# Kernel tuning notes

Measured on AMD Instinct MI355X. Metric: run time of the kernel, lower is better.

## Reference

```python
import jax, jax.numpy as jnp
import numpy as np

TOP_K = 2
POOL = 4  # EfficientSpatialRouter.pool_scale


def silu(v):
    return v * jax.nn.sigmoid(v)


def setup_inputs() -> dict:
    key = jax.random.key(0)
    ks = jax.random.split(key, 6)
    B, C, H, W = 16, 256, 56, 56
    E, O = 4, 256
    hidden = 2 * C            # SimpleExpert expand_ratio=2
    red = max(C // 8, 8)      # router reduced_channels
    x = jax.random.normal(ks[0], (B, C, H, W), jnp.float32)
    router_w1 = jax.random.normal(ks[1], (red, C, 3, 3), jnp.float32) * 0.02
    router_w2 = jax.random.normal(ks[2], (E, red), jnp.float32) * 0.01
    expert_w1 = jax.random.normal(ks[3], (E, hidden, C), jnp.float32) * 0.05
    expert_w2 = jax.random.normal(ks[4], (E, O, hidden), jnp.float32) * 0.03
    shared_w = jax.random.normal(ks[5], (O, C), jnp.float32) * 0.05
    return {"x": x, "router_w1": router_w1, "router_w2": router_w2,
            "expert_w1": expert_w1, "expert_w2": expert_w2, "shared_w": shared_w}


def reference(x, router_w1, router_w2, expert_w1, expert_w2, shared_w):
    # Eval mode: no router noise; BatchNorm with default running stats
    # (mean=0, var=1, gamma=1, beta=0) is the identity, so BNs are omitted.
    B, C, H, W = x.shape
    E = router_w2.shape[0]

    # --- EfficientSpatialRouter ---
    xp = x.reshape(B, C, H // POOL, POOL, W // POOL, POOL).mean(axis=(3, 5))
    h = jax.lax.conv_general_dilated(
        xp, router_w1, window_strides=(1, 1), padding=((1, 1), (1, 1)),
        dimension_numbers=("NCHW", "OIHW", "NCHW"))
    h = silu(h)  # [B, red, H/4, W/4]
    # 1x1 conv to E channels then spatial mean == mean of per-pixel logits
    logits = jnp.einsum("er,brij->be", router_w2, h) / (h.shape[2] * h.shape[3])
    probs = jax.nn.softmax(logits, axis=1)
    topv, topi = jax.lax.top_k(probs, TOP_K)          # [B,k]
    topv = topv / (topv.sum(axis=1, keepdims=True) + 1e-6)

    # --- shared expert (1x1 conv + BN(id) + SiLU) ---
    shared = silu(jnp.einsum("oc,bcij->boij", shared_w, x))

    # --- all SimpleExperts densely (1x1 conv -> SiLU -> 1x1 conv) ---
    hid = silu(jnp.einsum("edc,bcij->bedij", expert_w1, x))   # [B,E,hid,H,W]
    eo = jnp.einsum("eod,bedij->beoij", expert_w2, hid)       # [B,E,O,H,W]

    # --- weighted combine of top-k experts ---
    wdense = jnp.zeros((B, E), x.dtype).at[jnp.arange(B)[:, None], topi].add(topv)
    expert_out = jnp.einsum("be,beoij->boij", wdense, eo)
    return shared + expert_out
```

## Files before the change

### kernel.cpp

```cpp
#include <hip/hip_runtime.h>
#include <hip/hip_bf16.h>

typedef __attribute__((ext_vector_type(8))) short bf16x8;
typedef __attribute__((ext_vector_type(16))) float f32x16;
typedef __attribute__((ext_vector_type(4))) unsigned short ushort4v;

static __device__ __forceinline__ unsigned short f2bf(float f) {
  unsigned u = __float_as_uint(f);
  return (unsigned short)((u + 0x7FFFu + ((u >> 16) & 1u)) >> 16);
}
static __device__ __forceinline__ float silu_f(float v) { return v / (1.f + __expf(-v)); }

#define MFMA32(a, b, c) __builtin_amdgcn_mfma_f32_32x32x16_bf16((a), (b), (c), 0, 0, 0)

__global__ void prep_k(const float* __restrict__ shw, const float* __restrict__ ew1,
                       const float* __restrict__ ew2, const float* __restrict__ x,
                       unsigned short* __restrict__ wshp, unsigned short* __restrict__ w1p,
                       unsigned short* __restrict__ w2p, float* __restrict__ xp) {
  const int bid = blockIdx.x;
  if (bid < 4352) {
    int idx = bid * 256 + threadIdx.x;
    if (idx < 65536) {
      int j = idx;
      int i = j & 7, l = (j >> 3) & 63, ks = (j >> 9) & 15, rb = j >> 13;
      int row = rb * 32 + (l & 31), k = ks * 16 + (l >> 5) * 8 + i;
      wshp[j] = f2bf(shw[row * 256 + k]);
    } else if (idx < 589824) {
      int j = idx - 65536;
      int i = j & 7, l = (j >> 3) & 63, ks = (j >> 9) & 15, rb = (j >> 13) & 15, e = j >> 17;
      int row = rb * 32 + (l & 31), k = ks * 16 + (l >> 5) * 8 + i;
      w1p[j] = f2bf(ew1[((size_t)e * 512 + row) * 256 + k]);
    } else if (idx < 1114112) {
      int j = idx - 589824;
      int i = j & 7, l = (j >> 3) & 63, ks = (j >> 9) & 31, rb = (j >> 14) & 7, e = j >> 17;
      int row = rb * 32 + (l & 31), k = ks * 16 + (l >> 5) * 8 + i;
      w2p[j] = f2bf(ew2[((size_t)e * 256 + row) * 512 + k]);
    }
  } else {
    int idx = (bid - 4352) * 256 + threadIdx.x;
    if (idx >= 16 * 256 * 196) return;
    int pj = idx % 14, tmp = idx / 14, pi = tmp % 14, bc = tmp / 14;
    const float* src = x + (size_t)bc * 3136 + pi * 4 * 56 + pj * 4;
    float s = 0.f;
#pragma unroll
    for (int u = 0; u < 4; ++u) {
      float4 v = *reinterpret_cast<const float4*>(src + u * 56);
      s += v.x + v.y + v.z + v.w;
    }
    xp[idx] = s * 0.0625f;
  }
}

__global__ __launch_bounds__(256) void router_conv_k(const float* __restrict__ xp,
                                                     const float* __restrict__ rw1,
                                                     float* __restrict__ hsum) {
  const int b = blockIdx.x >> 5, r = blockIdx.x & 31;
  __shared__ float wl[2304];
  __shared__ float xl[32][256];
  __shared__ float red[4][196];
  __shared__ float red2[4];
  const int t = threadIdx.x;
  const int w = t >> 6, l = t & 63;
  for (int i = t; i < 2304; i += 256) wl[i] = rw1[r * 2304 + i];
  for (int i = t; i < 32 * 256; i += 256) (&xl[0][0])[i] = 0.f;
  const int ui = (l < 49) ? (l / 7) : 0, uj = (l < 49) ? (l % 7) : 0;
  float acc[4] = {0.f, 0.f, 0.f, 0.f};
  for (int cc = 0; cc < 8; ++cc) {
    __syncthreads();
    for (int i = t; i < 32 * 196; i += 256) {
      int c = i / 196, px = i % 196;
      xl[c][(px / 14 + 1) * 16 + (px % 14 + 1)] =
          xp[((size_t)b * 256 + cc * 32 + c) * 196 + px];
    }
    __syncthreads();
    if (l < 49) {
#pragma unroll 2
      for (int ci = 0; ci < 8; ++ci) {
        const int c = w * 8 + ci;
        float xv[4][4];
        const float* xb = &xl[c][ui * 32 + uj * 2];
#pragma unroll
        for (int dr = 0; dr < 4; ++dr)
#pragma unroll
          for (int dc = 0; dc < 4; ++dc) xv[dr][dc] = xb[dr * 16 + dc];
        const float* wp = &wl[(cc * 32 + c) * 9];
        float wv[9];
#pragma unroll
        for (int j = 0; j < 9; ++j) wv[j] = wp[j];
#pragma unroll
        for (int di = 0; di < 2; ++di)
#pragma unroll
          for (int dj = 0; dj < 2; ++dj) {
            float a = acc[di * 2 + dj];
#pragma unroll
            for (int du = 0; du < 3; ++du)
#pragma unroll
              for (int dv = 0; dv < 3; ++dv)
                a += xv[di + du][dj + dv] * wv[du * 3 + dv];
            acc[di * 2 + dj] = a;
          }
      }
    }
  }
  if (l < 49) {
#pragma unroll
    for (int k = 0; k < 4; ++k) red[w][(ui * 7 + uj) * 4 + k] = acc[k];
  }
  __syncthreads();
  float s = 0.f;
  if (t < 196) {
    float tot = red[0][t] + red[1][t] + red[2][t] + red[3][t];
    s = silu_f(tot);
  }
#pragma unroll
  for (int off = 32; off > 0; off >>= 1) s += __shfl_down(s, off);
  if ((t & 63) == 0) red2[t >> 6] = s;
  __syncthreads();
  if (t == 0) hsum[b * 32 + r] = red2[0] + red2[1] + red2[2] + red2[3];
}

__global__ void topk_k(const float* __restrict__ hsum, const float* __restrict__ rw2,
                       float* __restrict__ selv, int* __restrict__ sele) {
  const int t = threadIdx.x;
  const int b = t >> 2, e = t & 3;
  float l = 0.f;
#pragma unroll
  for (int r = 0; r < 32; ++r) l += rw2[e * 32 + r] * hsum[b * 32 + r];
  l *= (1.f / 196.f);
  float m = fmaxf(l, __shfl_xor(l, 1));
  m = fmaxf(m, __shfl_xor(m, 2));
  float p = __expf(l - m);
  float sm = p + __shfl_xor(p, 1);
  sm += __shfl_xor(sm, 2);
  float prob = p / sm;
  float p0 = __shfl(prob, (b << 2) | 0);
  float p1 = __shfl(prob, (b << 2) | 1);
  float p2 = __shfl(prob, (b << 2) | 2);
  float p3 = __shfl(prob, (b << 2) | 3);
  if (e == 0) {
    float pr[4] = {p0, p1, p2, p3};
    int i1 = 0;
    for (int i = 1; i < 4; ++i)
      if (pr[i] > pr[i1]) i1 = i;
    int i2 = (i1 == 0) ? 1 : 0;
    for (int i = 0; i < 4; ++i) {
      if (i == i1 || i == i2) continue;
      if (pr[i] > pr[i2]) i2 = i;
    }
    float denom = pr[i1] + pr[i2] + 1e-6f;
    selv[b * 2 + 0] = pr[i1] / denom;
    selv[b * 2 + 1] = pr[i2] / denom;
    sele[b * 2 + 0] = i1;
    sele[b * 2 + 1] = i2;
  }
}

template <int NKS>
static __device__ __forceinline__ void gemm_rf2(
    const unsigned short* __restrict__ A0, const unsigned short* __restrict__ A1,
    const unsigned short* B0, const unsigned short* B1, f32x16 acc[2][2]) {
#pragma unroll
  for (int kk = 0; kk < NKS; ++kk) {
    const bf16x8 a0 = *reinterpret_cast<const bf16x8*>(A0 + kk * 512);
    const bf16x8 a1 = *reinterpret_cast<const bf16x8*>(A1 + kk * 512);
    const bf16x8 b0 = *reinterpret_cast<const bf16x8*>(B0 + kk * 1024);
    const bf16x8 b1 = *reinterpret_cast<const bf16x8*>(B1 + kk * 1024);
    acc[0][0] = MFMA32(a0, b0, acc[0][0]);
    acc[0][1] = MFMA32(a0, b1, acc[0][1]);
    acc[1][0] = MFMA32(a1, b0, acc[1][0]);
    acc[1][1] = MFMA32(a1, b1, acc[1][1]);
  }
}

__global__ __launch_bounds__(256, 2) void moe_main_k(
    const float* __restrict__ x, const unsigned short* __restrict__ wshp,
    const unsigned short* __restrict__ w1p, const unsigned short* __restrict__ w2p,
    const float* __restrict__ selv, const int* __restrict__ sele,
    float* __restrict__ out) {
  constexpr int HW = 3136;
  __shared__ __align__(16) unsigned short xs[32 * 64 * 8];
  __shared__ __align__(16) unsigned short hs[2][16 * 64 * 8];

  const int b = blockIdx.x / 49, tile = blockIdx.x - b * 49;
  const int px0 = tile * 64;
  const int t = threadIdx.x;
  const int w = t >> 6, l = t & 63;
  const int l31 = l & 31, lh = l >> 5;

  {
    const float* xb = x + (size_t)b * 256 * HW + px0 + l;
#pragma unroll
    for (int cg = 0; cg < 8; ++cg) {
      const int c0 = w * 64 + cg * 8;
      alignas(16) unsigned short tmp[8];
#pragma unroll
      for (int i = 0; i < 8; ++i) tmp[i] = f2bf(xb[(size_t)(c0 + i) * HW]);
      *reinterpret_cast<bf16x8*>(&xs[((c0 >> 3) * 64 + l) * 8]) =
          *reinterpret_cast<const bf16x8*>(tmp);
    }
  }

  const unsigned short* xB0 = xs + (lh * 64 + l31) * 8;
  const unsigned short* xB1 = xB0 + 256;

  const int e0 = sele[b * 2 + 0], e1 = sele[b * 2 + 1];
  const float v0 = selv[b * 2 + 0], v1 = selv[b * 2 + 1];

  f32x16 oacc[2][2];
  f32x16 hacc[2];
#pragma unroll
  for (int i = 0; i < 2; ++i)
#pragma unroll
    for (int j = 0; j < 2; ++j)
#pragma unroll
      for (int r = 0; r < 16; ++r) oacc[i][j][r] = 0.f;
#pragma unroll
  for (int j = 0; j < 2; ++j)
#pragma unroll
    for (int r = 0; r < 16; ++r) hacc[j][r] = 0.f;

  __syncthreads();

  {
    const unsigned short* A1 = w1p + (size_t)((e0 * 16 + w) * 16) * 512 + l * 8;
    const unsigned short* As = wshp + (size_t)(w * 2) * 16 * 512 + l * 8;
#pragma unroll
    for (int kk = 0; kk < 16; ++kk) {
      const bf16x8 a1 = *reinterpret_cast<const bf16x8*>(A1 + kk * 512);
      const bf16x8 s0 = *reinterpret_cast<const bf16x8*>(As + kk * 512);
      const bf16x8 s1 = *reinterpret_cast<const bf16x8*>(As + 8192 + kk * 512);
      const bf16x8 b0 = *reinterpret_cast<const bf16x8*>(xB0 + kk * 1024);
      const bf16x8 b1 = *reinterpret_cast<const bf16x8*>(xB1 + kk * 1024);
      hacc[0] = MFMA32(a1, b0, hacc[0]);
      hacc[1] = MFMA32(a1, b1, hacc[1]);
      oacc[0][0] = MFMA32(s0, b0, oacc[0][0]);
      oacc[0][1] = MFMA32(s0, b1, oacc[0][1]);
      oacc[1][0] = MFMA32(s1, b0, oacc[1][0]);
      oacc[1][1] = MFMA32(s1, b1, oacc[1][1]);
    }
  }
#pragma unroll
  for (int i = 0; i < 2; ++i)
#pragma unroll
    for (int j = 0; j < 2; ++j)
#pragma unroll
      for (int r = 0; r < 16; ++r) oacc[i][j][r] = silu_f(oacc[i][j][r]);

#pragma unroll
  for (int cf = 0; cf < 2; ++cf)
#pragma unroll
    for (int g = 0; g < 4; ++g) {
      alignas(8) unsigned short pk[4];
#pragma unroll
      for (int j = 0; j < 4; ++j) pk[j] = f2bf(v0 * silu_f(hacc[cf][g * 4 + j]));
      const int ui2 = ((w * 4 + g) * 64 + cf * 32 + l31) * 8 + lh * 4;
      *reinterpret_cast<ushort4v*>(&hs[0][ui2]) = *reinterpret_cast<const ushort4v*>(pk);
    }
  __syncthreads();

#pragma unroll 1
  for (int p = 1; p < 8; ++p) {
    const int e = (p >> 2) ? e1 : e0, ch = p & 3;
    const int ep = ((p - 1) >> 2) ? e1 : e0, chp = (p - 1) & 3;
    const float v = (p >> 2) ? v1 : v0;
    const unsigned short* A1 = w1p + (size_t)((e * 16 + ch * 4 + w) * 16) * 512 + l * 8;
    const unsigned short* A2 = w2p + ((size_t)(ep * 8 + w * 2) * 32 + chp * 8) * 512 + l * 8;
    const unsigned short* B2 = hs[(p - 1) & 1] + (lh * 64 + l31) * 8;
#pragma unroll
    for (int j = 0; j < 2; ++j)
#pragma unroll
      for (int r = 0; r < 16; ++r) hacc[j][r] = 0.f;
#pragma unroll
    for (int kk = 0; kk < 16; ++kk) {
      const bf16x8 a1 = *reinterpret_cast<const bf16x8*>(A1 + kk * 512);
      const bf16x8 b0 = *reinterpret_cast<const bf16x8*>(xB0 + kk * 1024);
      const bf16x8 b1 = *reinterpret_cast<const bf16x8*>(xB1 + kk * 1024);
      hacc[0] = MFMA32(a1, b0, hacc[0]);
      hacc[1] = MFMA32(a1, b1, hacc[1]);
      if ((kk & 1) == 0) {
        const int ks2 = kk >> 1;
        const bf16x8 a20 = *reinterpret_cast<const bf16x8*>(A2 + ks2 * 512);
        const bf16x8 a21 = *reinterpret_cast<const bf16x8*>(A2 + 16384 + ks2 * 512);
        const bf16x8 h0 = *reinterpret_cast<const bf16x8*>(B2 + ks2 * 1024);
        const bf16x8 h1 = *reinterpret_cast<const bf16x8*>(B2 + 256 + ks2 * 1024);
        oacc[0][0] = MFMA32(a20, h0, oacc[0][0]);
        oacc[0][1] = MFMA32(a20, h1, oacc[0][1]);
        oacc[1][0] = MFMA32(a21, h0, oacc[1][0]);
        oacc[1][1] = MFMA32(a21, h1, oacc[1][1]);
      }
    }
#pragma unroll
    for (int cf = 0; cf < 2; ++cf)
#pragma unroll
      for (int g = 0; g < 4; ++g) {
        alignas(8) unsigned short pk[4];
#pragma unroll
        for (int j = 0; j < 4; ++j) pk[j] = f2bf(v * silu_f(hacc[cf][g * 4 + j]));
        const int ui2 = ((w * 4 + g) * 64 + cf * 32 + l31) * 8 + lh * 4;
        *reinterpret_cast<ushort4v*>(&hs[p & 1][ui2]) =
            *reinterpret_cast<const ushort4v*>(pk);
      }
    __syncthreads();
  }

  {
    const unsigned short* A2 = w2p + ((size_t)(e1 * 8 + w * 2) * 32 + 3 * 8) * 512 + l * 8;
    const unsigned short* B2 = hs[1] + (lh * 64 + l31) * 8;
    gemm_rf2<8>(A2, A2 + 16384, B2, B2 + 256, oacc);
  }

#pragma unroll
  for (int rfi = 0; rfi < 2; ++rfi)
#pragma unroll
    for (int cf = 0; cf < 2; ++cf)
#pragma unroll
      for (int r = 0; r < 16; ++r) {
        const int o = w * 64 + rfi * 32 + (r & 3) + 8 * (r >> 2) + 4 * lh;
        out[((size_t)b * 256 + o) * HW + px0 + cf * 32 + l31] = oacc[rfi][cf][r];
      }
}

extern "C" void kernel_launch(void* const* d_in, const int* in_sizes, int n_in,
                              void* d_out, int out_size, void* d_ws, size_t ws_size,
                              hipStream_t stream) {
  const float* x = (const float*)d_in[0];
  const float* rw1 = (const float*)d_in[1];
  const float* rw2 = (const float*)d_in[2];
  const float* ew1 = (const float*)d_in[3];
  const float* ew2 = (const float*)d_in[4];
  const float* shw = (const float*)d_in[5];
  float* out = (float*)d_out;
  char* ws = (char*)d_ws;

  float* xp = (float*)(ws);
  float* hsum = (float*)(ws + 3211264);
  float* selv = (float*)(ws + 3213312);
  int* sele = (int*)(ws + 3213440);
  unsigned short* wshp = (unsigned short*)(ws + 3213568);
  unsigned short* w1p = wshp + 65536;
  unsigned short* w2p = w1p + 524288;

  prep_k<<<7488, 256, 0, stream>>>(shw, ew1, ew2, x, wshp, w1p, w2p, xp);
  router_conv_k<<<512, 256, 0, stream>>>(xp, rw1, hsum);
  topk_k<<<1, 64, 0, stream>>>(hsum, rw2, selv, sele);
  moe_main_k<<<784, 256, 0, stream>>>(x, wshp, w1p, w2p, selv, sele, out);
}
```

Measured before the change: 188.7 us.

## Warp-specialize MoE main kernel into producer and consumer wave groups

Splits the four waves of each block into two roles. Two producer waves compute the expert hidden activations (first expert GEMM plus SiLU) into a single shared buffer. Two consumer waves compute the shared expert and accumulate the second expert GEMM over a 128-row output slice, and the two groups hand off through paired barriers. It also raises launch bounds to 3 blocks per SM, halves the hidden LDS buffer, and adds s_setprio around MFMA bursts. The intent is to overlap the two GEMM stages across waves and raise occupancy, at the cost of larger per-wave accumulators (register pressure) and a possible load imbalance between the roles.

```diff
diff --git a/kernel.cpp b/kernel.cpp
--- a/kernel.cpp
+++ b/kernel.cpp
@@ -155,31 +155,14 @@
   }
 }
 
-template <int NKS>
-static __device__ __forceinline__ void gemm_rf2(
-    const unsigned short* __restrict__ A0, const unsigned short* __restrict__ A1,
-    const unsigned short* B0, const unsigned short* B1, f32x16 acc[2][2]) {
-#pragma unroll
-  for (int kk = 0; kk < NKS; ++kk) {
-    const bf16x8 a0 = *reinterpret_cast<const bf16x8*>(A0 + kk * 512);
-    const bf16x8 a1 = *reinterpret_cast<const bf16x8*>(A1 + kk * 512);
-    const bf16x8 b0 = *reinterpret_cast<const bf16x8*>(B0 + kk * 1024);
-    const bf16x8 b1 = *reinterpret_cast<const bf16x8*>(B1 + kk * 1024);
-    acc[0][0] = MFMA32(a0, b0, acc[0][0]);
-    acc[0][1] = MFMA32(a0, b1, acc[0][1]);
-    acc[1][0] = MFMA32(a1, b0, acc[1][0]);
-    acc[1][1] = MFMA32(a1, b1, acc[1][1]);
-  }
-}
-
-__global__ __launch_bounds__(256, 2) void moe_main_k(
+__global__ __launch_bounds__(256, 3) void moe_main_k(
     const float* __restrict__ x, const unsigned short* __restrict__ wshp,
     const unsigned short* __restrict__ w1p, const unsigned short* __restrict__ w2p,
     const float* __restrict__ selv, const int* __restrict__ sele,
     float* __restrict__ out) {
   constexpr int HW = 3136;
   __shared__ __align__(16) unsigned short xs[32 * 64 * 8];
-  __shared__ __align__(16) unsigned short hs[2][16 * 64 * 8];
+  __shared__ __align__(16) unsigned short hs[16 * 64 * 8];
 
   const int b = blockIdx.x / 49, tile = blockIdx.x - b * 49;
   const int px0 = tile * 64;
@@ -202,122 +185,161 @@
 
   const unsigned short* xB0 = xs + (lh * 64 + l31) * 8;
   const unsigned short* xB1 = xB0 + 256;
+  const unsigned short* hB0 = hs + (lh * 64 + l31) * 8;
+  const unsigned short* hB1 = hB0 + 256;
 
   const int e0 = sele[b * 2 + 0], e1 = sele[b * 2 + 1];
   const float v0 = selv[b * 2 + 0], v1 = selv[b * 2 + 1];
 
-  f32x16 oacc[2][2];
-  f32x16 hacc[2];
-#pragma unroll
-  for (int i = 0; i < 2; ++i)
-#pragma unroll
-    for (int j = 0; j < 2; ++j)
-#pragma unroll
-      for (int r = 0; r < 16; ++r) oacc[i][j][r] = 0.f;
-#pragma unroll
-  for (int j = 0; j < 2; ++j)
-#pragma unroll
-    for (int r = 0; r < 16; ++r) hacc[j][r] = 0.f;
-
   __syncthreads();
 
-  {
-    const unsigned short* A1 = w1p + (size_t)((e0 * 16 + w) * 16) * 512 + l * 8;
-    const unsigned short* As = wshp + (size_t)(w * 2) * 16 * 512 + l * 8;
-#pragma unroll
-    for (int kk = 0; kk < 16; ++kk) {
-      const bf16x8 a1 = *reinterpret_cast<const bf16x8*>(A1 + kk * 512);
-      const bf16x8 s0 = *reinterpret_cast<const bf16x8*>(As + kk * 512);
-      const bf16x8 s1 = *reinterpret_cast<const bf16x8*>(As + 8192 + kk * 512);
-      const bf16x8 b0 = *reinterpret_cast<const bf16x8*>(xB0 + kk * 1024);
-      const bf16x8 b1 = *reinterpret_cast<const bf16x8*>(xB1 + kk * 1024);
-      hacc[0] = MFMA32(a1, b0, hacc[0]);
-      hacc[1] = MFMA32(a1, b1, hacc[1]);
-      oacc[0][0] = MFMA32(s0, b0, oacc[0][0]);
-      oacc[0][1] = MFMA32(s0, b1, oacc[0][1]);
-      oacc[1][0] = MFMA32(s1, b0, oacc[1][0]);
-      oacc[1][1] = MFMA32(s1, b1, oacc[1][1]);
-    }
-  }
-#pragma unroll
-  for (int i = 0; i < 2; ++i)
-#pragma unroll
-    for (int j = 0; j < 2; ++j)
-#pragma unroll
-      for (int r = 0; r < 16; ++r) oacc[i][j][r] = silu_f(oacc[i][j][r]);
-
-#pragma unroll
-  for (int cf = 0; cf < 2; ++cf)
-#pragma unroll
-    for (int g = 0; g < 4; ++g) {
-      alignas(8) unsigned short pk[4];
-#pragma unroll
-      for (int j = 0; j < 4; ++j) pk[j] = f2bf(v0 * silu_f(hacc[cf][g * 4 + j]));
-      const int ui2 = ((w * 4 + g) * 64 + cf * 32 + l31) * 8 + lh * 4;
-      *reinterpret_cast<ushort4v*>(&hs[0][ui2]) = *reinterpret_cast<const ushort4v*>(pk);
-    }
-  __syncthreads();
-
+  if (w < 2) {
+    f32x16 hacc[2][2];
 #pragma unroll 1
-  for (int p = 1; p < 8; ++p) {
-    const int e = (p >> 2) ? e1 : e0, ch = p & 3;
-    const int ep = ((p - 1) >> 2) ? e1 : e0, chp = (p - 1) & 3;
-    const float v = (p >> 2) ? v1 : v0;
-    const unsigned short* A1 = w1p + (size_t)((e * 16 + ch * 4 + w) * 16) * 512 + l * 8;
-    const unsigned short* A2 = w2p + ((size_t)(ep * 8 + w * 2) * 32 + chp * 8) * 512 + l * 8;
-    const unsigned short* B2 = hs[(p - 1) & 1] + (lh * 64 + l31) * 8;
-#pragma unroll
-    for (int j = 0; j < 2; ++j)
-#pragma unroll
-      for (int r = 0; r < 16; ++r) hacc[j][r] = 0.f;
-#pragma unroll
-    for (int kk = 0; kk < 16; ++kk) {
-      const bf16x8 a1 = *reinterpret_cast<const bf16x8*>(A1 + kk * 512);
-      const bf16x8 b0 = *reinterpret_cast<const bf16x8*>(xB0 + kk * 1024);
-      const bf16x8 b1 = *reinterpret_cast<const bf16x8*>(xB1 + kk * 1024);
-      hacc[0] = MFMA32(a1, b0, hacc[0]);
-      hacc[1] = MFMA32(a1, b1, hacc[1]);
-      if ((kk & 1) == 0) {
-        const int ks2 = kk >> 1;
-        const bf16x8 a20 = *reinterpret_cast<const bf16x8*>(A2 + ks2 * 512);
-        const bf16x8 a21 = *reinterpret_cast<const bf16x8*>(A2 + 16384 + ks2 * 512);
-        const bf16x8 h0 = *reinterpret_cast<const bf16x8*>(B2 + ks2 * 1024);
-        const bf16x8 h1 = *reinterpret_cast<const bf16x8*>(B2 + 256 + ks2 * 1024);
-        oacc[0][0] = MFMA32(a20, h0, oacc[0][0]);
-        oacc[0][1] = MFMA32(a20, h1, oacc[0][1]);
-        oacc[1][0] = MFMA32(a21, h0, oacc[1][0]);
-        oacc[1][1] = MFMA32(a21, h1, oacc[1][1]);
-      }
-    }
-#pragma unroll
-    for (int cf = 0; cf < 2; ++cf)
-#pragma unroll
-      for (int g = 0; g < 4; ++g) {
-        alignas(8) unsigned short pk[4];
-#pragma unroll
-        for (int j = 0; j < 4; ++j) pk[j] = f2bf(v * silu_f(hacc[cf][g * 4 + j]));
-        const int ui2 = ((w * 4 + g) * 64 + cf * 32 + l31) * 8 + lh * 4;
-        *reinterpret_cast<ushort4v*>(&hs[p & 1][ui2]) =
-            *reinterpret_cast<const ushort4v*>(pk);
-      }
+    for (int p = 0; p < 8; ++p) {
+      const int e = (p >> 2) ? e1 : e0;
+      const float v = (p >> 2) ? v1 : v0;
+      const unsigned short* A1 =
+          w1p + (size_t)((e * 16 + (p & 3) * 4 + w * 2) * 16) * 512 + l * 8;
+#pragma unroll
+      for (int i = 0; i < 2; ++i)
+#pragma unroll
+        for (int j = 0; j < 2; ++j)
+#pragma unroll
+          for (int r = 0; r < 16; ++r) hacc[i][j][r] = 0.f;
+#pragma unroll
+      for (int kk = 0; kk < 16; ++kk) {
+        const bf16x8 a0 = *reinterpret_cast<const bf16x8*>(A1 + kk * 512);
+        const bf16x8 a1 = *reinterpret_cast<const bf16x8*>(A1 + 8192 + kk * 512);
+        const bf16x8 b0 = *reinterpret_cast<const bf16x8*>(xB0 + kk * 1024);
+        const bf16x8 b1 = *reinterpret_cast<const bf16x8*>(xB1 + kk * 1024);
+        __builtin_amdgcn_s_setprio(1);
+        hacc[0][0] = MFMA32(a0, b0, hacc[0][0]);
+        hacc[0][1] = MFMA32(a0, b1, hacc[0][1]);
+        hacc[1][0] = MFMA32(a1, b0, hacc[1][0]);
+        hacc[1][1] = MFMA32(a1, b1, hacc[1][1]);
+        __builtin_amdgcn_s_setprio(0);
+      }
+      ushort4v pk[2][2][4];
+#pragma unroll
+      for (int rfi = 0; rfi < 2; ++rfi)
+#pragma unroll
+        for (int cf = 0; cf < 2; ++cf)
+#pragma unroll
+          for (int g = 0; g < 4; ++g) {
+            alignas(8) unsigned short tmp[4];
+#pragma unroll
+            for (int j = 0; j < 4; ++j)
+              tmp[j] = f2bf(v * silu_f(hacc[rfi][cf][g * 4 + j]));
+            pk[rfi][cf][g] = *reinterpret_cast<const ushort4v*>(tmp);
+          }
+      __syncthreads();
+#pragma unroll
+      for (int rfi = 0; rfi < 2; ++rfi)
+#pragma unroll
+        for (int cf = 0; cf < 2; ++cf)
+#pragma unroll
+          for (int g = 0; g < 4; ++g) {
+            const int kg = w * 8 + rfi * 4 + g;
+            const int ui2 = (kg * 64 + cf * 32 + l31) * 8 + lh * 4;
+            *reinterpret_cast<ushort4v*>(&hs[ui2]) = pk[rfi][cf][g];
+          }
+      __syncthreads();
+    }
+  } else {
+    const int wc = w - 2;
+    f32x16 oacc[4][2];
+#pragma unroll
+    for (int i = 0; i < 4; ++i)
+#pragma unroll
+      for (int j = 0; j < 2; ++j)
+#pragma unroll
+        for (int r = 0; r < 16; ++r) oacc[i][j][r] = 0.f;
+
+    {
+      const unsigned short* As = wshp + (size_t)((wc * 4) * 16) * 512 + l * 8;
+#pragma unroll
+      for (int kk = 0; kk < 16; ++kk) {
+        bf16x8 a[4];
+#pragma unroll
+        for (int rr = 0; rr < 4; ++rr)
+          a[rr] = *reinterpret_cast<const bf16x8*>(As + rr * 8192 + kk * 512);
+        const bf16x8 b0 = *reinterpret_cast<const bf16x8*>(xB0 + kk * 1024);
+        const bf16x8 b1 = *reinterpret_cast<const bf16x8*>(xB1 + kk * 1024);
+        __builtin_amdgcn_s_setprio(1);
+#pragma unroll
+        for (int rr = 0; rr < 4; ++rr) {
+          oacc[rr][0] = MFMA32(a[rr], b0, oacc[rr][0]);
+          oacc[rr][1] = MFMA32(a[rr], b1, oacc[rr][1]);
+        }
+        __builtin_amdgcn_s_setprio(0);
+      }
+    }
+#pragma unroll
+    for (int i = 0; i < 4; ++i)
+#pragma unroll
+      for (int j = 0; j < 2; ++j)
+#pragma unroll
+        for (int r = 0; r < 16; ++r) oacc[i][j][r] = silu_f(oacc[i][j][r]);
+
     __syncthreads();
-  }
-
-  {
-    const unsigned short* A2 = w2p + ((size_t)(e1 * 8 + w * 2) * 32 + 3 * 8) * 512 + l * 8;
-    const unsigned short* B2 = hs[1] + (lh * 64 + l31) * 8;
-    gemm_rf2<8>(A2, A2 + 16384, B2, B2 + 256, oacc);
-  }
-
-#pragma unroll
-  for (int rfi = 0; rfi < 2; ++rfi)
-#pragma unroll
-    for (int cf = 0; cf < 2; ++cf)
-#pragma unroll
-      for (int r = 0; r < 16; ++r) {
-        const int o = w * 64 + rfi * 32 + (r & 3) + 8 * (r >> 2) + 4 * lh;
-        out[((size_t)b * 256 + o) * HW + px0 + cf * 32 + l31] = oacc[rfi][cf][r];
-      }
+    __syncthreads();
+
+#pragma unroll 1
+    for (int p = 1; p < 8; ++p) {
+      const int q = p - 1;
+      const int e = (q >> 2) ? e1 : e0;
+      const unsigned short* A2 =
+          w2p + ((size_t)(e * 8 + wc * 4) * 32 + (q & 3) * 8) * 512 + l * 8;
+#pragma unroll
+      for (int kk = 0; kk < 8; ++kk) {
+        bf16x8 a[4];
+#pragma unroll
+        for (int rr = 0; rr < 4; ++rr)
+          a[rr] = *reinterpret_cast<const bf16x8*>(A2 + rr * 16384 + kk * 512);
+        const bf16x8 h0 = *reinterpret_cast<const bf16x8*>(hB0 + kk * 1024);
+        const bf16x8 h1 = *reinterpret_cast<const bf16x8*>(hB1 + kk * 1024);
+        __builtin_amdgcn_s_setprio(1);
+#pragma unroll
+        for (int rr = 0; rr < 4; ++rr) {
+          oacc[rr][0] = MFMA32(a[rr], h0, oacc[rr][0]);
+          oacc[rr][1] = MFMA32(a[rr], h1, oacc[rr][1]);
+        }
+        __builtin_amdgcn_s_setprio(0);
+      }
+      __syncthreads();
+      __syncthreads();
+    }
+
+    {
+      const unsigned short* A2 =
+          w2p + ((size_t)(e1 * 8 + wc * 4) * 32 + 3 * 8) * 512 + l * 8;
+#pragma unroll
+      for (int kk = 0; kk < 8; ++kk) {
+        bf16x8 a[4];
+#pragma unroll
+        for (int rr = 0; rr < 4; ++rr)
+          a[rr] = *reinterpret_cast<const bf16x8*>(A2 + rr * 16384 + kk * 512);
+        const bf16x8 h0 = *reinterpret_cast<const bf16x8*>(hB0 + kk * 1024);
+        const bf16x8 h1 = *reinterpret_cast<const bf16x8*>(hB1 + kk * 1024);
+#pragma unroll
+        for (int rr = 0; rr < 4; ++rr) {
+          oacc[rr][0] = MFMA32(a[rr], h0, oacc[rr][0]);
+          oacc[rr][1] = MFMA32(a[rr], h1, oacc[rr][1]);
+        }
+      }
+    }
+
+#pragma unroll
+    for (int rr = 0; rr < 4; ++rr)
+#pragma unroll
+      for (int cf = 0; cf < 2; ++cf)
+#pragma unroll
+        for (int r = 0; r < 16; ++r) {
+          const int o = wc * 128 + rr * 32 + (r & 3) + 8 * (r >> 2) + 4 * lh;
+          out[((size_t)b * 256 + o) * HW + px0 + cf * 32 + l31] = oacc[rr][cf][r];
+        }
+  }
 }
 
 extern "C" void kernel_launch(void* const* d_in, const int* in_sizes, int n_in,
```

After: 247.7 us. 1.31x slower.

## Hold x fragments in registers, alias smem, and software-pipeline weight loads

Applied to the files above, without the earlier changes.

Loads the block's whole bf16 x tile from LDS into registers once (32 bf16x8 fragments per lane), so the x staging buffer can be reused as the hidden buffer and shared memory drops to 32KB. The pipeline that overlapped GEMM1 of one phase with GEMM2 of the previous phase through a double-buffered hs is replaced by sequential GEMM1 then GEMM2 per phase. Each phase now has an extra barrier, and weight loads are explicitly prefetched with s_setprio and sched_barrier hints. The large register footprint risks spilling or lower occupancy under launch_bounds(256,2), and the cross-phase overlap is lost.

```diff
diff --git a/kernel.cpp b/kernel.cpp
--- a/kernel.cpp
+++ b/kernel.cpp
@@ -155,31 +155,15 @@
   }
 }
 
-template <int NKS>
-static __device__ __forceinline__ void gemm_rf2(
-    const unsigned short* __restrict__ A0, const unsigned short* __restrict__ A1,
-    const unsigned short* B0, const unsigned short* B1, f32x16 acc[2][2]) {
-#pragma unroll
-  for (int kk = 0; kk < NKS; ++kk) {
-    const bf16x8 a0 = *reinterpret_cast<const bf16x8*>(A0 + kk * 512);
-    const bf16x8 a1 = *reinterpret_cast<const bf16x8*>(A1 + kk * 512);
-    const bf16x8 b0 = *reinterpret_cast<const bf16x8*>(B0 + kk * 1024);
-    const bf16x8 b1 = *reinterpret_cast<const bf16x8*>(B1 + kk * 1024);
-    acc[0][0] = MFMA32(a0, b0, acc[0][0]);
-    acc[0][1] = MFMA32(a0, b1, acc[0][1]);
-    acc[1][0] = MFMA32(a1, b0, acc[1][0]);
-    acc[1][1] = MFMA32(a1, b1, acc[1][1]);
-  }
-}
-
 __global__ __launch_bounds__(256, 2) void moe_main_k(
     const float* __restrict__ x, const unsigned short* __restrict__ wshp,
     const unsigned short* __restrict__ w1p, const unsigned short* __restrict__ w2p,
     const float* __restrict__ selv, const int* __restrict__ sele,
     float* __restrict__ out) {
   constexpr int HW = 3136;
-  __shared__ __align__(16) unsigned short xs[32 * 64 * 8];
-  __shared__ __align__(16) unsigned short hs[2][16 * 64 * 8];
+  __shared__ __align__(16) unsigned short smem[16384];
+  unsigned short* xs = smem;
+  unsigned short* hs = smem;
 
   const int b = blockIdx.x / 49, tile = blockIdx.x - b * 49;
   const int px0 = tile * 64;
@@ -200,43 +184,47 @@
     }
   }
 
-  const unsigned short* xB0 = xs + (lh * 64 + l31) * 8;
-  const unsigned short* xB1 = xB0 + 256;
-
   const int e0 = sele[b * 2 + 0], e1 = sele[b * 2 + 1];
   const float v0 = selv[b * 2 + 0], v1 = selv[b * 2 + 1];
 
+  __syncthreads();
+
+  bf16x8 xf[16][2];
+  {
+    const unsigned short* xB0 = xs + (lh * 64 + l31) * 8;
+#pragma unroll
+    for (int kk = 0; kk < 16; ++kk) {
+      xf[kk][0] = *reinterpret_cast<const bf16x8*>(xB0 + kk * 1024);
+      xf[kk][1] = *reinterpret_cast<const bf16x8*>(xB0 + 256 + kk * 1024);
+    }
+  }
+
   f32x16 oacc[2][2];
-  f32x16 hacc[2];
 #pragma unroll
   for (int i = 0; i < 2; ++i)
 #pragma unroll
     for (int j = 0; j < 2; ++j)
 #pragma unroll
       for (int r = 0; r < 16; ++r) oacc[i][j][r] = 0.f;
-#pragma unroll
-  for (int j = 0; j < 2; ++j)
-#pragma unroll
-    for (int r = 0; r < 16; ++r) hacc[j][r] = 0.f;
-
-  __syncthreads();
 
   {
-    const unsigned short* A1 = w1p + (size_t)((e0 * 16 + w) * 16) * 512 + l * 8;
     const unsigned short* As = wshp + (size_t)(w * 2) * 16 * 512 + l * 8;
+    bf16x8 s0r[2], s1r[2];
+    s0r[0] = *reinterpret_cast<const bf16x8*>(As);
+    s1r[0] = *reinterpret_cast<const bf16x8*>(As + 8192);
 #pragma unroll
     for (int kk = 0; kk < 16; ++kk) {
-      const bf16x8 a1 = *reinterpret_cast<const bf16x8*>(A1 + kk * 512);
-      const bf16x8 s0 = *reinterpret_cast<const bf16x8*>(As + kk * 512);
-      const bf16x8 s1 = *reinterpret_cast<const bf16x8*>(As + 8192 + kk * 512);
-      const bf16x8 b0 = *reinterpret_cast<const bf16x8*>(xB0 + kk * 1024);
-      const bf16x8 b1 = *reinterpret_cast<const bf16x8*>(xB1 + kk * 1024);
-      hacc[0] = MFMA32(a1, b0, hacc[0]);
-      hacc[1] = MFMA32(a1, b1, hacc[1]);
-      oacc[0][0] = MFMA32(s0, b0, oacc[0][0]);
-      oacc[0][1] = MFMA32(s0, b1, oacc[0][1]);
-      oacc[1][0] = MFMA32(s1, b0, oacc[1][0]);
-      oacc[1][1] = MFMA32(s1, b1, oacc[1][1]);
+      const int cur = kk & 1, nxt = cur ^ 1;
+      if (kk < 15) {
+        s0r[nxt] = *reinterpret_cast<const bf16x8*>(As + (kk + 1) * 512);
+        s1r[nxt] = *reinterpret_cast<const bf16x8*>(As + 8192 + (kk + 1) * 512);
+      }
+      __builtin_amdgcn_s_setprio(1);
+      oacc[0][0] = MFMA32(s0r[cur], xf[kk][0], oacc[0][0]);
+      oacc[0][1] = MFMA32(s0r[cur], xf[kk][1], oacc[0][1]);
+      oacc[1][0] = MFMA32(s1r[cur], xf[kk][0], oacc[1][0]);
+      oacc[1][1] = MFMA32(s1r[cur], xf[kk][1], oacc[1][1]);
+      __builtin_amdgcn_s_setprio(0);
     }
   }
 #pragma unroll
@@ -246,67 +234,81 @@
 #pragma unroll
       for (int r = 0; r < 16; ++r) oacc[i][j][r] = silu_f(oacc[i][j][r]);
 
-#pragma unroll
-  for (int cf = 0; cf < 2; ++cf)
-#pragma unroll
-    for (int g = 0; g < 4; ++g) {
-      alignas(8) unsigned short pk[4];
-#pragma unroll
-      for (int j = 0; j < 4; ++j) pk[j] = f2bf(v0 * silu_f(hacc[cf][g * 4 + j]));
-      const int ui2 = ((w * 4 + g) * 64 + cf * 32 + l31) * 8 + lh * 4;
-      *reinterpret_cast<ushort4v*>(&hs[0][ui2]) = *reinterpret_cast<const ushort4v*>(pk);
-    }
-  __syncthreads();
-
 #pragma unroll 1
-  for (int p = 1; p < 8; ++p) {
+  for (int p = 0; p < 8; ++p) {
     const int e = (p >> 2) ? e1 : e0, ch = p & 3;
-    const int ep = ((p - 1) >> 2) ? e1 : e0, chp = (p - 1) & 3;
     const float v = (p >> 2) ? v1 : v0;
-    const unsigned short* A1 = w1p + (size_t)((e * 16 + ch * 4 + w) * 16) * 512 + l * 8;
-    const unsigned short* A2 = w2p + ((size_t)(ep * 8 + w * 2) * 32 + chp * 8) * 512 + l * 8;
-    const unsigned short* B2 = hs[(p - 1) & 1] + (lh * 64 + l31) * 8;
+
+    f32x16 hacc[2];
 #pragma unroll
     for (int j = 0; j < 2; ++j)
 #pragma unroll
       for (int r = 0; r < 16; ++r) hacc[j][r] = 0.f;
-#pragma unroll
-    for (int kk = 0; kk < 16; ++kk) {
-      const bf16x8 a1 = *reinterpret_cast<const bf16x8*>(A1 + kk * 512);
-      const bf16x8 b0 = *reinterpret_cast<const bf16x8*>(xB0 + kk * 1024);
-      const bf16x8 b1 = *reinterpret_cast<const bf16x8*>(xB1 + kk * 1024);
-      hacc[0] = MFMA32(a1, b0, hacc[0]);
-      hacc[1] = MFMA32(a1, b1, hacc[1]);
-      if ((kk & 1) == 0) {
-        const int ks2 = kk >> 1;
-        const bf16x8 a20 = *reinterpret_cast<const bf16x8*>(A2 + ks2 * 512);
-        const bf16x8 a21 = *reinterpret_cast<const bf16x8*>(A2 + 16384 + ks2 * 512);
-        const bf16x8 h0 = *reinterpret_cast<const bf16x8*>(B2 + ks2 * 1024);
-        const bf16x8 h1 = *reinterpret_cast<const bf16x8*>(B2 + 256 + ks2 * 1024);
-        oacc[0][0] = MFMA32(a20, h0, oacc[0][0]);
-        oacc[0][1] = MFMA32(a20, h1, oacc[0][1]);
-        oacc[1][0] = MFMA32(a21, h0, oacc[1][0]);
-        oacc[1][1] = MFMA32(a21, h1, oacc[1][1]);
-      }
-    }
+    {
+      const unsigned short* A1 =
+          w1p + (size_t)((e * 16 + ch * 4 + w) * 16) * 512 + l * 8;
+      bf16x8 ar[3];
+      ar[0] = *reinterpret_cast<const bf16x8*>(A1);
+      ar[1] = *reinterpret_cast<const bf16x8*>(A1 + 512);
+#pragma unroll
+      for (int kk = 0; kk < 16; ++kk) {
+        const int s = kk % 3;
+        if (kk < 14)
+          ar[(kk + 2) % 3] = *reinterpret_cast<const bf16x8*>(A1 + (kk + 2) * 512);
+        __builtin_amdgcn_sched_barrier(0);
+        __builtin_amdgcn_s_setprio(1);
+        hacc[0] = MFMA32(ar[s], xf[kk][0], hacc[0]);
+        hacc[1] = MFMA32(ar[s], xf[kk][1], hacc[1]);
+        __builtin_amdgcn_s_setprio(0);
+      }
+    }
+    ushort4v pk[2][4];
 #pragma unroll
     for (int cf = 0; cf < 2; ++cf)
 #pragma unroll
       for (int g = 0; g < 4; ++g) {
-        alignas(8) unsigned short pk[4];
-#pragma unroll
-        for (int j = 0; j < 4; ++j) pk[j] = f2bf(v * silu_f(hacc[cf][g * 4 + j]));
+        alignas(8) unsigned short tmp[4];
+#pragma unroll
+        for (int j = 0; j < 4; ++j) tmp[j] = f2bf(v * silu_f(hacc[cf][g * 4 + j]));
+        pk[cf][g] = *reinterpret_cast<const ushort4v*>(tmp);
+      }
+
+    __syncthreads();
+#pragma unroll
+    for (int cf = 0; cf < 2; ++cf)
+#pragma unroll
+      for (int g = 0; g < 4; ++g) {
         const int ui2 = ((w * 4 + g) * 64 + cf * 32 + l31) * 8 + lh * 4;
-        *reinterpret_cast<ushort4v*>(&hs[p & 1][ui2]) =
-            *reinterpret_cast<const ushort4v*>(pk);
+        *reinterpret_cast<ushort4v*>(&hs[ui2]) = pk[cf][g];
       }
     __syncthreads();
-  }
-
-  {
-    const unsigned short* A2 = w2p + ((size_t)(e1 * 8 + w * 2) * 32 + 3 * 8) * 512 + l * 8;
-    const unsigned short* B2 = hs[1] + (lh * 64 + l31) * 8;
-    gemm_rf2<8>(A2, A2 + 16384, B2, B2 + 256, oacc);
+
+    {
+      const unsigned short* A2 =
+          w2p + ((size_t)(e * 8 + w * 2) * 32 + ch * 8) * 512 + l * 8;
+      const unsigned short* hB0 = hs + (lh * 64 + l31) * 8;
+      bf16x8 a0r[2], a1r[2], h0r[2], h1r[2];
+      a0r[0] = *reinterpret_cast<const bf16x8*>(A2);
+      a1r[0] = *reinterpret_cast<const bf16x8*>(A2 + 16384);
+      h0r[0] = *reinterpret_cast<const bf16x8*>(hB0);
+      h1r[0] = *reinterpret_cast<const bf16x8*>(hB0 + 256);
+#pragma unroll
+      for (int kk = 0; kk < 8; ++kk) {
+        const int cur = kk & 1, nxt = cur ^ 1;
+        if (kk < 7) {
+          a0r[nxt] = *reinterpret_cast<const bf16x8*>(A2 + (kk + 1) * 512);
+          a1r[nxt] = *reinterpret_cast<const bf16x8*>(A2 + 16384 + (kk + 1) * 512);
+          h0r[nxt] = *reinterpret_cast<const bf16x8*>(hB0 + (kk + 1) * 1024);
+          h1r[nxt] = *reinterpret_cast<const bf16x8*>(hB0 + 256 + (kk + 1) * 1024);
+        }
+        __builtin_amdgcn_s_setprio(1);
+        oacc[0][0] = MFMA32(a0r[cur], h0r[cur], oacc[0][0]);
+        oacc[0][1] = MFMA32(a0r[cur], h1r[cur], oacc[0][1]);
+        oacc[1][0] = MFMA32(a1r[cur], h0r[cur], oacc[1][0]);
+        oacc[1][1] = MFMA32(a1r[cur], h1r[cur], oacc[1][1]);
+        __builtin_amdgcn_s_setprio(0);
+      }
+    }
   }
 
 #pragma unroll
```

New measurement: 176.0 us. -6.7%, faster.

## Warp-specialize MoE kernel into producer/consumer waves and double-buffer router conv

Applied to the files above, without the earlier changes.

The main MoE kernel now runs 512 threads. Four waves produce expert hidden activations (first GEMM plus SiLU) into double-buffered LDS, and four other waves compute the shared expert and consume the hidden tiles for the second GEMM. Both sides are kept in step by matching barrier counts. The inner loops gain register prefetch of the next operands and s_setprio around MFMAs. The router conv is restructured to prefetch the next 16-channel chunk into a second LDS buffer while computing the current one. The aim is to overlap the two GEMM stages and hide load latency, at the cost of higher register and LDS pressure and strict barrier pairing between the wave groups.

```diff
diff --git a/kernel.cpp b/kernel.cpp
--- a/kernel.cpp
+++ b/kernel.cpp
@@ -56,34 +56,40 @@
                                                      float* __restrict__ hsum) {
   const int b = blockIdx.x >> 5, r = blockIdx.x & 31;
   __shared__ float wl[2304];
-  __shared__ float xl[32][256];
+  __shared__ float xl[2][16][256];
   __shared__ float red[4][196];
   __shared__ float red2[4];
   const int t = threadIdx.x;
   const int w = t >> 6, l = t & 63;
   for (int i = t; i < 2304; i += 256) wl[i] = rw1[r * 2304 + i];
-  for (int i = t; i < 32 * 256; i += 256) (&xl[0][0])[i] = 0.f;
+  for (int i = t; i < 2 * 16 * 256; i += 256) (&xl[0][0][0])[i] = 0.f;
   const int ui = (l < 49) ? (l / 7) : 0, uj = (l < 49) ? (l % 7) : 0;
   float acc[4] = {0.f, 0.f, 0.f, 0.f};
-  for (int cc = 0; cc < 8; ++cc) {
-    __syncthreads();
-    for (int i = t; i < 32 * 196; i += 256) {
-      int c = i / 196, px = i % 196;
-      xl[c][(px / 14 + 1) * 16 + (px % 14 + 1)] =
-          xp[((size_t)b * 256 + cc * 32 + c) * 196 + px];
-    }
-    __syncthreads();
+  for (int i = t; i < 16 * 196; i += 256) {
+    int c = i / 196, px = i % 196;
+    xl[0][c][(px / 14 + 1) * 16 + (px % 14 + 1)] = xp[((size_t)b * 256 + c) * 196 + px];
+  }
+  __syncthreads();
+  for (int cc = 0; cc < 16; ++cc) {
+    if (cc < 15) {
+      for (int i = t; i < 16 * 196; i += 256) {
+        int c = i / 196, px = i % 196;
+        xl[(cc + 1) & 1][c][(px / 14 + 1) * 16 + (px % 14 + 1)] =
+            xp[((size_t)b * 256 + (cc + 1) * 16 + c) * 196 + px];
+      }
+    }
     if (l < 49) {
-#pragma unroll 2
-      for (int ci = 0; ci < 8; ++ci) {
-        const int c = w * 8 + ci;
+      const float(*xb_buf)[256] = xl[cc & 1];
+#pragma unroll
+      for (int ci = 0; ci < 4; ++ci) {
+        const int c = w * 4 + ci;
         float xv[4][4];
-        const float* xb = &xl[c][ui * 32 + uj * 2];
+        const float* xb = &xb_buf[c][ui * 32 + uj * 2];
 #pragma unroll
         for (int dr = 0; dr < 4; ++dr)
 #pragma unroll
           for (int dc = 0; dc < 4; ++dc) xv[dr][dc] = xb[dr * 16 + dc];
-        const float* wp = &wl[(cc * 32 + c) * 9];
+        const float* wp = &wl[(cc * 16 + c) * 9];
         float wv[9];
 #pragma unroll
         for (int j = 0; j < 9; ++j) wv[j] = wp[j];
@@ -101,6 +107,7 @@
           }
       }
     }
+    __syncthreads();
   }
   if (l < 49) {
 #pragma unroll
@@ -155,24 +162,7 @@
   }
 }
 
-template <int NKS>
-static __device__ __forceinline__ void gemm_rf2(
-    const unsigned short* __restrict__ A0, const unsigned short* __restrict__ A1,
-    const unsigned short* B0, const unsigned short* B1, f32x16 acc[2][2]) {
-#pragma unroll
-  for (int kk = 0; kk < NKS; ++kk) {
-    const bf16x8 a0 = *reinterpret_cast<const bf16x8*>(A0 + kk * 512);
-    const bf16x8 a1 = *reinterpret_cast<const bf16x8*>(A1 + kk * 512);
-    const bf16x8 b0 = *reinterpret_cast<const bf16x8*>(B0 + kk * 1024);
-    const bf16x8 b1 = *reinterpret_cast<const bf16x8*>(B1 + kk * 1024);
-    acc[0][0] = MFMA32(a0, b0, acc[0][0]);
-    acc[0][1] = MFMA32(a0, b1, acc[0][1]);
-    acc[1][0] = MFMA32(a1, b0, acc[1][0]);
-    acc[1][1] = MFMA32(a1, b1, acc[1][1]);
-  }
-}
-
-__global__ __launch_bounds__(256, 2) void moe_main_k(
+__global__ __launch_bounds__(512, 4) void moe_main_k(
     const float* __restrict__ x, const unsigned short* __restrict__ wshp,
     const unsigned short* __restrict__ w1p, const unsigned short* __restrict__ w2p,
     const float* __restrict__ selv, const int* __restrict__ sele,
@@ -190,8 +180,8 @@
   {
     const float* xb = x + (size_t)b * 256 * HW + px0 + l;
 #pragma unroll
-    for (int cg = 0; cg < 8; ++cg) {
-      const int c0 = w * 64 + cg * 8;
+    for (int cg = 0; cg < 4; ++cg) {
+      const int c0 = w * 32 + cg * 8;
       alignas(16) unsigned short tmp[8];
 #pragma unroll
       for (int i = 0; i < 8; ++i) tmp[i] = f2bf(xb[(size_t)(c0 + i) * HW]);
@@ -200,124 +190,177 @@
     }
   }
 
+  const int e0 = sele[b * 2 + 0], e1 = sele[b * 2 + 1];
+  const float v0 = selv[b * 2 + 0], v1 = selv[b * 2 + 1];
+
   const unsigned short* xB0 = xs + (lh * 64 + l31) * 8;
   const unsigned short* xB1 = xB0 + 256;
 
-  const int e0 = sele[b * 2 + 0], e1 = sele[b * 2 + 1];
-  const float v0 = selv[b * 2 + 0], v1 = selv[b * 2 + 1];
-
-  f32x16 oacc[2][2];
-  f32x16 hacc[2];
-#pragma unroll
-  for (int i = 0; i < 2; ++i)
-#pragma unroll
-    for (int j = 0; j < 2; ++j)
-#pragma unroll
-      for (int r = 0; r < 16; ++r) oacc[i][j][r] = 0.f;
-#pragma unroll
-  for (int j = 0; j < 2; ++j)
-#pragma unroll
-    for (int r = 0; r < 16; ++r) hacc[j][r] = 0.f;
-
   __syncthreads();
 
-  {
-    const unsigned short* A1 = w1p + (size_t)((e0 * 16 + w) * 16) * 512 + l * 8;
-    const unsigned short* As = wshp + (size_t)(w * 2) * 16 * 512 + l * 8;
-#pragma unroll
-    for (int kk = 0; kk < 16; ++kk) {
-      const bf16x8 a1 = *reinterpret_cast<const bf16x8*>(A1 + kk * 512);
-      const bf16x8 s0 = *reinterpret_cast<const bf16x8*>(As + kk * 512);
-      const bf16x8 s1 = *reinterpret_cast<const bf16x8*>(As + 8192 + kk * 512);
-      const bf16x8 b0 = *reinterpret_cast<const bf16x8*>(xB0 + kk * 1024);
-      const bf16x8 b1 = *reinterpret_cast<const bf16x8*>(xB1 + kk * 1024);
-      hacc[0] = MFMA32(a1, b0, hacc[0]);
-      hacc[1] = MFMA32(a1, b1, hacc[1]);
-      oacc[0][0] = MFMA32(s0, b0, oacc[0][0]);
-      oacc[0][1] = MFMA32(s0, b1, oacc[0][1]);
-      oacc[1][0] = MFMA32(s1, b0, oacc[1][0]);
-      oacc[1][1] = MFMA32(s1, b1, oacc[1][1]);
-    }
-  }
-#pragma unroll
-  for (int i = 0; i < 2; ++i)
-#pragma unroll
-    for (int j = 0; j < 2; ++j)
-#pragma unroll
-      for (int r = 0; r < 16; ++r) oacc[i][j][r] = silu_f(oacc[i][j][r]);
-
-#pragma unroll
-  for (int cf = 0; cf < 2; ++cf)
-#pragma unroll
-    for (int g = 0; g < 4; ++g) {
-      alignas(8) unsigned short pk[4];
-#pragma unroll
-      for (int j = 0; j < 4; ++j) pk[j] = f2bf(v0 * silu_f(hacc[cf][g * 4 + j]));
-      const int ui2 = ((w * 4 + g) * 64 + cf * 32 + l31) * 8 + lh * 4;
-      *reinterpret_cast<ushort4v*>(&hs[0][ui2]) = *reinterpret_cast<const ushort4v*>(pk);
-    }
-  __syncthreads();
-
+  if (w < 4) {
+    f32x16 hacc[2];
+    {
+      const unsigned short* A1 = w1p + (size_t)((e0 * 16 + w) * 16) * 512 + l * 8;
+#pragma unroll
+      for (int j = 0; j < 2; ++j)
+#pragma unroll
+        for (int r = 0; r < 16; ++r) hacc[j][r] = 0.f;
+      bf16x8 aC = *reinterpret_cast<const bf16x8*>(A1);
+      bf16x8 b0C = *reinterpret_cast<const bf16x8*>(xB0);
+      bf16x8 b1C = *reinterpret_cast<const bf16x8*>(xB1);
+#pragma unroll
+      for (int kk = 0; kk < 16; ++kk) {
+        bf16x8 aN, b0N, b1N;
+        if (kk < 15) {
+          aN = *reinterpret_cast<const bf16x8*>(A1 + (kk + 1) * 512);
+          b0N = *reinterpret_cast<const bf16x8*>(xB0 + (kk + 1) * 1024);
+          b1N = *reinterpret_cast<const bf16x8*>(xB1 + (kk + 1) * 1024);
+        }
+        __builtin_amdgcn_s_setprio(1);
+        hacc[0] = MFMA32(aC, b0C, hacc[0]);
+        hacc[1] = MFMA32(aC, b1C, hacc[1]);
+        __builtin_amdgcn_s_setprio(0);
+        aC = aN; b0C = b0N; b1C = b1N;
+      }
+#pragma unroll
+      for (int cf = 0; cf < 2; ++cf)
+#pragma unroll
+        for (int g = 0; g < 4; ++g) {
+          alignas(8) unsigned short pk[4];
+#pragma unroll
+          for (int j = 0; j < 4; ++j) pk[j] = f2bf(v0 * silu_f(hacc[cf][g * 4 + j]));
+          const int ui2 = ((w * 4 + g) * 64 + cf * 32 + l31) * 8 + lh * 4;
+          *reinterpret_cast<ushort4v*>(&hs[0][ui2]) = *reinterpret_cast<const ushort4v*>(pk);
+        }
+    }
+    __syncthreads();
 #pragma unroll 1
-  for (int p = 1; p < 8; ++p) {
-    const int e = (p >> 2) ? e1 : e0, ch = p & 3;
-    const int ep = ((p - 1) >> 2) ? e1 : e0, chp = (p - 1) & 3;
-    const float v = (p >> 2) ? v1 : v0;
-    const unsigned short* A1 = w1p + (size_t)((e * 16 + ch * 4 + w) * 16) * 512 + l * 8;
-    const unsigned short* A2 = w2p + ((size_t)(ep * 8 + w * 2) * 32 + chp * 8) * 512 + l * 8;
-    const unsigned short* B2 = hs[(p - 1) & 1] + (lh * 64 + l31) * 8;
-#pragma unroll
-    for (int j = 0; j < 2; ++j)
-#pragma unroll
-      for (int r = 0; r < 16; ++r) hacc[j][r] = 0.f;
-#pragma unroll
-    for (int kk = 0; kk < 16; ++kk) {
-      const bf16x8 a1 = *reinterpret_cast<const bf16x8*>(A1 + kk * 512);
-      const bf16x8 b0 = *reinterpret_cast<const bf16x8*>(xB0 + kk * 1024);
-      const bf16x8 b1 = *reinterpret_cast<const bf16x8*>(xB1 + kk * 1024);
-      hacc[0] = MFMA32(a1, b0, hacc[0]);
-      hacc[1] = MFMA32(a1, b1, hacc[1]);
-      if ((kk & 1) == 0) {
-        const int ks2 = kk >> 1;
-        const bf16x8 a20 = *reinterpret_cast<const bf16x8*>(A2 + ks2 * 512);
-        const bf16x8 a21 = *reinterpret_cast<const bf16x8*>(A2 + 16384 + ks2 * 512);
-        const bf16x8 h0 = *reinterpret_cast<const bf16x8*>(B2 + ks2 * 1024);
-        const bf16x8 h1 = *reinterpret_cast<const bf16x8*>(B2 + 256 + ks2 * 1024);
-        oacc[0][0] = MFMA32(a20, h0, oacc[0][0]);
-        oacc[0][1] = MFMA32(a20, h1, oacc[0][1]);
-        oacc[1][0] = MFMA32(a21, h0, oacc[1][0]);
-        oacc[1][1] = MFMA32(a21, h1, oacc[1][1]);
-      }
-    }
-#pragma unroll
-    for (int cf = 0; cf < 2; ++cf)
-#pragma unroll
-      for (int g = 0; g < 4; ++g) {
-        alignas(8) unsigned short pk[4];
-#pragma unroll
-        for (int j = 0; j < 4; ++j) pk[j] = f2bf(v * silu_f(hacc[cf][g * 4 + j]));
-        const int ui2 = ((w * 4 + g) * 64 + cf * 32 + l31) * 8 + lh * 4;
-        *reinterpret_cast<ushort4v*>(&hs[p & 1][ui2]) =
-            *reinterpret_cast<const ushort4v*>(pk);
-      }
+    for (int q = 0; q < 8; ++q) {
+      if (q < 7) {
+        const int p = q + 1;
+        const int e = (p >> 2) ? e1 : e0, ch = p & 3;
+        const float v = (p >> 2) ? v1 : v0;
+        const unsigned short* A1 =
+            w1p + (size_t)((e * 16 + ch * 4 + w) * 16) * 512 + l * 8;
+#pragma unroll
+        for (int j = 0; j < 2; ++j)
+#pragma unroll
+          for (int r = 0; r < 16; ++r) hacc[j][r] = 0.f;
+        bf16x8 aC = *reinterpret_cast<const bf16x8*>(A1);
+        bf16x8 b0C = *reinterpret_cast<const bf16x8*>(xB0);
+        bf16x8 b1C = *reinterpret_cast<const bf16x8*>(xB1);
+#pragma unroll
+        for (int kk = 0; kk < 16; ++kk) {
+          bf16x8 aN, b0N, b1N;
+          if (kk < 15) {
+            aN = *reinterpret_cast<const bf16x8*>(A1 + (kk + 1) * 512);
+            b0N = *reinterpret_cast<const bf16x8*>(xB0 + (kk + 1) * 1024);
+            b1N = *reinterpret_cast<const bf16x8*>(xB1 + (kk + 1) * 1024);
+          }
+          __builtin_amdgcn_s_setprio(1);
+          hacc[0] = MFMA32(aC, b0C, hacc[0]);
+          hacc[1] = MFMA32(aC, b1C, hacc[1]);
+          __builtin_amdgcn_s_setprio(0);
+          aC = aN; b0C = b0N; b1C = b1N;
+        }
+#pragma unroll
+        for (int cf = 0; cf < 2; ++cf)
+#pragma unroll
+          for (int g = 0; g < 4; ++g) {
+            alignas(8) unsigned short pk[4];
+#pragma unroll
+            for (int j = 0; j < 4; ++j) pk[j] = f2bf(v * silu_f(hacc[cf][g * 4 + j]));
+            const int ui2 = ((w * 4 + g) * 64 + cf * 32 + l31) * 8 + lh * 4;
+            *reinterpret_cast<ushort4v*>(&hs[p & 1][ui2]) =
+                *reinterpret_cast<const ushort4v*>(pk);
+          }
+      }
+      __syncthreads();
+    }
+  } else {
+    const int wc = w - 4;
+    f32x16 oacc[2][2];
+#pragma unroll
+    for (int i = 0; i < 2; ++i)
+#pragma unroll
+      for (int j = 0; j < 2; ++j)
+#pragma unroll
+        for (int r = 0; r < 16; ++r) oacc[i][j][r] = 0.f;
+
+    {
+      const unsigned short* As = wshp + (size_t)(wc * 2) * 16 * 512 + l * 8;
+      bf16x8 a0C = *reinterpret_cast<const bf16x8*>(As);
+      bf16x8 a1C = *reinterpret_cast<const bf16x8*>(As + 8192);
+      bf16x8 b0C = *reinterpret_cast<const bf16x8*>(xB0);
+      bf16x8 b1C = *reinterpret_cast<const bf16x8*>(xB1);
+#pragma unroll
+      for (int kk = 0; kk < 16; ++kk) {
+        bf16x8 a0N, a1N, b0N, b1N;
+        if (kk < 15) {
+          a0N = *reinterpret_cast<const bf16x8*>(As + (kk + 1) * 512);
+          a1N = *reinterpret_cast<const bf16x8*>(As + 8192 + (kk + 1) * 512);
+          b0N = *reinterpret_cast<const bf16x8*>(xB0 + (kk + 1) * 1024);
+          b1N = *reinterpret_cast<const bf16x8*>(xB1 + (kk + 1) * 1024);
+        }
+        __builtin_amdgcn_s_setprio(1);
+        oacc[0][0] = MFMA32(a0C, b0C, oacc[0][0]);
+        oacc[0][1] = MFMA32(a0C, b1C, oacc[0][1]);
+        oacc[1][0] = MFMA32(a1C, b0C, oacc[1][0]);
+        oacc[1][1] = MFMA32(a1C, b1C, oacc[1][1]);
+        __builtin_amdgcn_s_setprio(0);
+        a0C = a0N; a1C = a1N; b0C = b0N; b1C = b1N;
+      }
+    }
+#pragma unroll
+    for (int i = 0; i < 2; ++i)
+#pragma unroll
+      for (int j = 0; j < 2; ++j)
+#pragma unroll
+        for (int r = 0; r < 16; ++r) oacc[i][j][r] = silu_f(oacc[i][j][r]);
+
     __syncthreads();
-  }
-
-  {
-    const unsigned short* A2 = w2p + ((size_t)(e1 * 8 + w * 2) * 32 + 3 * 8) * 512 + l * 8;
-    const unsigned short* B2 = hs[1] + (lh * 64 + l31) * 8;
-    gemm_rf2<8>(A2, A2 + 16384, B2, B2 + 256, oacc);
-  }
-
-#pragma unroll
-  for (int rfi = 0; rfi < 2; ++rfi)
-#pragma unroll
-    for (int cf = 0; cf < 2; ++cf)
-#pragma unroll
-      for (int r = 0; r < 16; ++r) {
-        const int o = w * 64 + rfi * 32 + (r & 3) + 8 * (r >> 2) + 4 * lh;
-        out[((size_t)b * 256 + o) * HW + px0 + cf * 32 + l31] = oacc[rfi][cf][r];
-      }
+#pragma unroll 1
+    for (int q = 0; q < 8; ++q) {
+      const int e = (q >> 2) ? e1 : e0, ch = q & 3;
+      const unsigned short* A2 =
+          w2p + ((size_t)(e * 8 + wc * 2) * 32 + ch * 8) * 512 + l * 8;
+      const unsigned short* hB0 = hs[q & 1] + (lh * 64 + l31) * 8;
+      const unsigned short* hB1 = hB0 + 256;
+      bf16x8 a0C = *reinterpret_cast<const bf16x8*>(A2);
+      bf16x8 a1C = *reinterpret_cast<const bf16x8*>(A2 + 16384);
+      bf16x8 h0C = *reinterpret_cast<const bf16x8*>(hB0);
+      bf16x8 h1C = *reinterpret_cast<const bf16x8*>(hB1);
+#pragma unroll
+      for (int kk = 0; kk < 8; ++kk) {
+        bf16x8 a0N, a1N, h0N, h1N;
+        if (kk < 7) {
+          a0N = *reinterpret_cast<const bf16x8*>(A2 + (kk + 1) * 512);
+          a1N = *reinterpret_cast<const bf16x8*>(A2 + 16384 + (kk + 1) * 512);
+          h0N = *reinterpret_cast<const bf16x8*>(hB0 + (kk + 1) * 1024);
+          h1N = *reinterpret_cast<const bf16x8*>(hB1 + (kk + 1) * 1024);
+        }
+        __builtin_amdgcn_s_setprio(1);
+        oacc[0][0] = MFMA32(a0C, h0C, oacc[0][0]);
+        oacc[0][1] = MFMA32(a0C, h1C, oacc[0][1]);
+        oacc[1][0] = MFMA32(a1C, h0C, oacc[1][0]);
+        oacc[1][1] = MFMA32(a1C, h1C, oacc[1][1]);
+        __builtin_amdgcn_s_setprio(0);
+        a0C = a0N; a1C = a1N; h0C = h0N; h1C = h1N;
+      }
+      __syncthreads();
+    }
+
+#pragma unroll
+    for (int rfi = 0; rfi < 2; ++rfi)
+#pragma unroll
+      for (int cf = 0; cf < 2; ++cf)
+#pragma unroll
+        for (int r = 0; r < 16; ++r) {
+          const int o = wc * 64 + rfi * 32 + (r & 3) + 8 * (r >> 2) + 4 * lh;
+          out[((size_t)b * 256 + o) * HW + px0 + cf * 32 + l31] = oacc[rfi][cf][r];
+        }
+  }
 }
 
 extern "C" void kernel_launch(void* const* d_in, const int* in_sizes, int n_in,
@@ -343,5 +386,5 @@
   prep_k<<<7488, 256, 0, stream>>>(shw, ew1, ew2, x, wshp, w1p, w2p, xp);
   router_conv_k<<<512, 256, 0, stream>>>(xp, rw1, hsum);
   topk_k<<<1, 64, 0, stream>>>(hsum, rw2, selv, sele);
-  moe_main_k<<<784, 256, 0, stream>>>(x, wshp, w1p, w2p, selv, sele, out);
-}
+  moe_main_k<<<784, 512, 0, stream>>>(x, wshp, w1p, w2p, selv, sele, out);
+}
```

Result: slower. 204.8 us (+8.5%).
